# Performance work log

Hardware: AMD Instinct MI355X
Metric: run time of the kernel (lower is better)

Reference implementation:

```python
import jax, jax.numpy as jnp
import numpy as np

N, D, H, O, E = 8192, 512, 2048, 512, 8

def setup_inputs() -> dict:
    key = jax.random.key(0)
    ks = jax.random.split(key, 7)
    s = lambda *sh: 1.0 / np.sqrt(sh[-2] if len(sh) > 1 else 1.0)
    x  = jax.random.normal(ks[0], (N, D), dtype=jnp.float32)
    Wr = jax.random.normal(ks[1], (D, E), dtype=jnp.float32) * (1.0 / np.sqrt(D))
    br = jnp.zeros((E,), dtype=jnp.float32)
    W1 = jax.random.normal(ks[2], (E, D, H), dtype=jnp.float32) * (1.0 / np.sqrt(D))
    b1 = jnp.zeros((E, H), dtype=jnp.float32)
    W2 = jax.random.normal(ks[3], (E, H, O), dtype=jnp.float32) * (1.0 / np.sqrt(H))
    b2 = jnp.zeros((E, O), dtype=jnp.float32)
    return {"x": x, "Wr": Wr, "br": br, "W1": W1, "b1": b1, "W2": W2, "b2": b2}


def reference(x, Wr, br, W1, b1, W2, b2):
    # --- supervised router step: Linear -> softmax -> max ---
    router_logits = x @ Wr + br                      # [N, E]
    router_probs = jax.nn.softmax(router_logits, axis=-1)
    p_max = jnp.max(router_probs, axis=-1)           # [N]
    routes = jnp.argmax(router_probs, axis=-1)       # [N] int
    onehot = jax.nn.one_hot(routes, W1.shape[0], dtype=x.dtype)  # [N, E] dispatch mask

    # --- per-expert MLP (dense reference for the gather/compute/scatter pattern) ---
    h = jax.nn.relu(jnp.einsum('nd,edh->enh', x, W1) + b1[:, None, :])  # [E, N, H]
    all_out = jnp.einsum('enh,eho->eno', h, W2) + b2[:, None, :]        # [E, N, O]

    # --- combine: each token takes its routed expert's output ---
    out = jnp.einsum('ne,eno->no', onehot, all_out)  # [N, O]

    # straight-through scaling: value 1 in fwd, routes gradient into router probs
    scale = p_max / jax.lax.stop_gradient(p_max)
    logits = out * scale[:, None]

    counts = jnp.sum(onehot, axis=0)                 # tokens per expert
    return logits, router_probs, counts
```

## Files before the change

kernel.cpp:

```cpp
#include <hip/hip_runtime.h>
#include <hip/hip_bf16.h>
#include <stdint.h>

#define N_TOK 8192
#define DIM   512
#define HID   2048
#define OUTD  512
#define NEXP  8

typedef short  bf16x8 __attribute__((ext_vector_type(8)));
typedef float  f32x4  __attribute__((ext_vector_type(4)));
typedef unsigned short u16x8 __attribute__((ext_vector_type(8)));
typedef unsigned short u16x4 __attribute__((ext_vector_type(4)));

#define WS_CNT    0
#define WS_LIST   4096
#define WS_XBF    266240
#define WS_W1T    8654848
#define WS_W2T    25432064
#define WS_H      42209280

__device__ __forceinline__ unsigned short f2bf(float f) {
    uint32_t u = __builtin_bit_cast(uint32_t, f);
    u = (u + 0x7fffu + ((u >> 16) & 1u)) >> 16;
    return (unsigned short)u;
}

__device__ __forceinline__ void gload16(const unsigned short* g, unsigned short* l) {
    __builtin_amdgcn_global_load_lds(
        (const __attribute__((address_space(1))) unsigned int*)g,
        (__attribute__((address_space(3))) unsigned int*)l, 16, 0, 0);
}

#define MFMA_BF16 __builtin_amdgcn_mfma_f32_16x16x32_bf16

__global__ __launch_bounds__(256) void prep_kernel(
    const float* __restrict__ x, const float* __restrict__ wr, const float* __restrict__ br,
    const float* __restrict__ w1, const float* __restrict__ w2,
    float* __restrict__ probs, int* __restrict__ cnt, int* __restrict__ list,
    unsigned short* __restrict__ xbf, unsigned short* __restrict__ w1t,
    unsigned short* __restrict__ w2t)
{
    const int bid = blockIdx.x, tid = threadIdx.x;
    if (bid < 128) {
        __shared__ int lcnt[NEXP], lbase[NEXP];
        __shared__ int am_l[64], slot_l[64];
        const int w = tid >> 6, lane = tid & 63;
        if (tid < NEXP) lcnt[tid] = 0;
        __syncthreads();
        for (int i = 0; i < 16; i++) {
            const int n = bid * 64 + w * 16 + i;
            float acc[NEXP] = {};
            #pragma unroll
            for (int db = 0; db < 8; db++) {
                const int d = db * 64 + lane;
                const float xv = x[(size_t)n * DIM + d];
                const f32x4 wv0 = *(const f32x4*)&wr[d * 8];
                const f32x4 wv1 = *(const f32x4*)&wr[d * 8 + 4];
                #pragma unroll
                for (int e = 0; e < 4; e++) { acc[e] += xv * wv0[e]; acc[4 + e] += xv * wv1[e]; }
            }
            #pragma unroll
            for (int m = 1; m < 64; m <<= 1)
                #pragma unroll
                for (int e = 0; e < NEXP; e++) acc[e] += __shfl_xor(acc[e], m, 64);
            #pragma unroll
            for (int e = 0; e < NEXP; e++) acc[e] += br[e];
            float mx = acc[0]; int am = 0;
            #pragma unroll
            for (int e = 1; e < NEXP; e++) if (acc[e] > mx) { mx = acc[e]; am = e; }
            float p[NEXP]; float s = 0.f;
            #pragma unroll
            for (int e = 0; e < NEXP; e++) { p[e] = expf(acc[e] - mx); s += p[e]; }
            const float inv = 1.f / s;
            if (lane == 0) {
                f32x4 p0, p1;
                #pragma unroll
                for (int e = 0; e < 4; e++) { p0[e] = p[e] * inv; p1[e] = p[e + 4] * inv; }
                *(f32x4*)&probs[(size_t)n * NEXP]     = p0;
                *(f32x4*)&probs[(size_t)n * NEXP + 4] = p1;
                const int slot = atomicAdd(&lcnt[am], 1);
                am_l[w * 16 + i] = am; slot_l[w * 16 + i] = slot;
            }
        }
        __syncthreads();
        if (tid < NEXP) lbase[tid] = atomicAdd(&cnt[tid], lcnt[tid]);
        __syncthreads();
        if (tid < 64) {
            const int a = am_l[tid];
            list[a * N_TOK + lbase[a] + slot_l[tid]] = bid * 64 + tid;
        }
    } else if (bid < 4224) {
        __shared__ float t[64][65];
        const float* pin; unsigned short* pout; int R, C, r0, c0;
        if (bid < 2176) {
            const int loc = bid - 128, e = loc >> 8, l2 = loc & 255;
            pin = w1 + (size_t)e * DIM * HID; pout = w1t + (size_t)e * DIM * HID;
            R = DIM; C = HID; r0 = (l2 >> 5) * 64; c0 = (l2 & 31) * 64;
        } else {
            const int loc = bid - 2176, e = loc >> 8, l2 = loc & 255;
            pin = w2 + (size_t)e * HID * OUTD; pout = w2t + (size_t)e * HID * OUTD;
            R = HID; C = OUTD; r0 = (l2 >> 3) * 64; c0 = (l2 & 7) * 64;
        }
        const int r = tid >> 2, q = tid & 3;
        #pragma unroll
        for (int j = 0; j < 4; j++) {
            f32x4 v = *(const f32x4*)&pin[(size_t)(r0 + r) * C + c0 + q * 16 + j * 4];
            #pragma unroll
            for (int i = 0; i < 4; i++) t[r][q * 16 + j * 4 + i] = v[i];
        }
        __syncthreads();
        unsigned short o[16];
        #pragma unroll
        for (int i = 0; i < 16; i++) o[i] = f2bf(t[q * 16 + i][r]);
        unsigned short* dst = &pout[(size_t)(c0 + r) * R + r0 + q * 16];
        *(u16x8*)dst       = *(const u16x8*)&o[0];
        *(u16x8*)(dst + 8) = *(const u16x8*)&o[8];
    } else {
        const size_t i = (size_t)(bid - 4224) * 256 + tid;
        f32x4 a = *(const f32x4*)&x[i * 8];
        f32x4 b = *(const f32x4*)&x[i * 8 + 4];
        u16x8 o;
        #pragma unroll
        for (int j = 0; j < 4; j++) { o[j] = f2bf(a[j]); o[4 + j] = f2bf(b[j]); }
        *(u16x8*)&xbf[i * 8] = o;
    }
}

__device__ __forceinline__ int xcd_swizzle(int bid, int nwg, bool& valid) {
    const int xcd = bid & 7, cidx = bid >> 3;
    const int q = nwg >> 3, r = nwg & 7;
    const int csz = q + (xcd < r ? 1 : 0);
    valid = (cidx < csz);
    return (xcd < r ? xcd * (q + 1) : r * (q + 1) + (xcd - r) * q) + cidx;
}

__device__ __forceinline__ void tile_map128(const int* __restrict__ cnt, int tile,
                                            int& e, int& row0, int& bs, int& m_e, int& ntiles) {
    int c[NEXP]; ntiles = 0;
    #pragma unroll
    for (int i = 0; i < NEXP; i++) { c[i] = cnt[i]; ntiles += (c[i] + 127) >> 7; }
    int t = tile, b = 0, ei = 0;
    #pragma unroll
    for (int i = 0; i < NEXP; i++) {
        const int nt = (c[i] + 127) >> 7;
        if (t >= 0 && t < nt) { ei = i; row0 = t << 7; bs = b; m_e = c[i]; }
        t -= nt; b += c[i];
    }
    e = ei;
}

__global__ __launch_bounds__(256) void gemm1_kernel(
    const unsigned short* __restrict__ xbf, const unsigned short* __restrict__ w1t,
    const float* __restrict__ b1, const int* __restrict__ list,
    const int* __restrict__ cnt, unsigned short* __restrict__ h)
{
    int e = 0, row0 = 0, bs = 0, m_e = 0, ntm = 0;
    tile_map128(cnt, 0, e, row0, bs, m_e, ntm);
    const int nwg = ntm * 32;
    bool valid; const int v = xcd_swizzle(blockIdx.x, nwg, valid);
    if (!valid) return;
    const int tile = v >> 5, ntile = v & 31;
    tile_map128(cnt, tile, e, row0, bs, m_e, ntm);
    const int n0 = ntile * 64;

    __shared__ unsigned short ldsA[128 * 64] __attribute__((aligned(16)));
    __shared__ unsigned short ldsB[64 * 64]  __attribute__((aligned(16)));
    __shared__ int ldsTok[128];
    const int tid = threadIdx.x;
    if (tid < 128) { int r = row0 + tid; if (r >= m_e) r = m_e - 1; ldsTok[tid] = list[e * N_TOK + r]; }
    __syncthreads();

    const int gslot = tid & 7;
    const unsigned short* aSrc[4]; const unsigned short* bSrc[2];
    #pragma unroll
    for (int i = 0; i < 4; i++) {
        const int row = (i * 256 + tid) >> 3;
        const int col = ((gslot ^ (row & 7)) << 3);
        aSrc[i] = xbf + (size_t)ldsTok[row] * DIM + col;
    }
    #pragma unroll
    for (int i = 0; i < 2; i++) {
        const int row = (i * 256 + tid) >> 3;
        const int col = ((gslot ^ (row & 7)) << 3);
        bSrc[i] = w1t + ((size_t)e * HID + n0 + row) * DIM + col;
    }

    f32x4 acc[4][2] = {};
    const int lane = tid & 63, wid = tid >> 6;
    const int wm = (wid >> 1) * 64, wn = (wid & 1) * 32;
    const int lrow = lane & 15, gk = lane >> 4, lm = lrow & 7;

    int rowA[4], rowB[2];
    #pragma unroll
    for (int f = 0; f < 4; f++) rowA[f] = (wm + f * 16 + lrow) * 64;
    #pragma unroll
    for (int f = 0; f < 2; f++) rowB[f] = (wn + f * 16 + lrow) * 64;

    for (int t = 0; t < 8; t++) {
        const int k0 = t * 64;
        __syncthreads();
        #pragma unroll
        for (int i = 0; i < 4; i++)
            gload16(aSrc[i] + k0, ldsA + ((i << 8) + (tid & 192)) * 8);
        #pragma unroll
        for (int i = 0; i < 2; i++)
            gload16(bSrc[i] + k0, ldsB + ((i << 8) + (tid & 192)) * 8);
        __syncthreads();
        #pragma unroll
        for (int kk = 0; kk < 2; kk++) {
            bf16x8 av[4], bv[2];
            #pragma unroll
            for (int f = 0; f < 4; f++)
                av[f] = *(const bf16x8*)&ldsA[rowA[f] + ((((kk << 2) + gk) ^ lm) << 3)];
            #pragma unroll
            for (int f = 0; f < 2; f++)
                bv[f] = *(const bf16x8*)&ldsB[rowB[f] + ((((kk << 2) + gk) ^ lm) << 3)];
            #pragma unroll
            for (int mf = 0; mf < 4; mf++)
                #pragma unroll
                for (int nf = 0; nf < 2; nf++)
                    acc[mf][nf] = MFMA_BF16(av[mf], bv[nf], acc[mf][nf], 0, 0, 0);
        }
    }

    const int hbase = bs + row0;
    float bias[2];
    #pragma unroll
    for (int nf = 0; nf < 2; nf++) bias[nf] = b1[e * HID + n0 + wn + nf * 16 + lrow];
    #pragma unroll
    for (int mf = 0; mf < 4; mf++) {
        #pragma unroll
        for (int j = 0; j < 4; j++) {
            const int m = wm + mf * 16 + gk * 4 + j;
            if (row0 + m < m_e) {
                const size_t ro = (size_t)(hbase + m) * HID + n0 + wn;
                #pragma unroll
                for (int nf = 0; nf < 2; nf++) {
                    float vv = acc[mf][nf][j] + bias[nf];
                    h[ro + nf * 16 + lrow] = f2bf(vv > 0.f ? vv : 0.f);
                }
            }
        }
    }
}

__global__ __launch_bounds__(256) void gemm2_kernel(
    const unsigned short* __restrict__ h, const unsigned short* __restrict__ w2t,
    const float* __restrict__ b2, const int* __restrict__ list,
    const int* __restrict__ cnt, float* __restrict__ out, float* __restrict__ counts)
{
    const int tid = threadIdx.x;
    if (blockIdx.x == 0 && tid < NEXP) counts[tid] = (float)cnt[tid];

    int e = 0, row0 = 0, bs = 0, m_e = 0, ntm = 0;
    tile_map128(cnt, 0, e, row0, bs, m_e, ntm);
    const int nwg = ntm * 8;
    bool valid; const int v = xcd_swizzle(blockIdx.x, nwg, valid);
    if (!valid) return;
    const int tile = v >> 3, ntile = v & 7;
    tile_map128(cnt, tile, e, row0, bs, m_e, ntm);
    const int n0 = ntile * 64;

    __shared__ unsigned short ldsA[128 * 64] __attribute__((aligned(16)));
    __shared__ unsigned short ldsB[64 * 64]  __attribute__((aligned(16)));
    __shared__ int ldsTok[128];
    if (tid < 128) { int r = row0 + tid; if (r >= m_e) r = m_e - 1; ldsTok[tid] = list[e * N_TOK + r]; }
    __syncthreads();

    const int gslot = tid & 7;
    const unsigned short* aSrc[4]; const unsigned short* bSrc[2];
    #pragma unroll
    for (int i = 0; i < 4; i++) {
        const int row = (i * 256 + tid) >> 3;
        const int col = ((gslot ^ (row & 7)) << 3);
        int slot = row0 + row; if (slot >= m_e) slot = m_e - 1;
        aSrc[i] = h + (size_t)(bs + slot) * HID + col;
    }
    #pragma unroll
    for (int i = 0; i < 2; i++) {
        const int row = (i * 256 + tid) >> 3;
        const int col = ((gslot ^ (row & 7)) << 3);
        bSrc[i] = w2t + ((size_t)e * OUTD + n0 + row) * HID + col;
    }

    f32x4 acc[4][2] = {};
    const int lane = tid & 63, wid = tid >> 6;
    const int wm = (wid >> 1) * 64, wn = (wid & 1) * 32;
    const int lrow = lane & 15, gk = lane >> 4, lm = lrow & 7;

    int rowA[4], rowB[2];
    #pragma unroll
    for (int f = 0; f < 4; f++) rowA[f] = (wm + f * 16 + lrow) * 64;
    #pragma unroll
    for (int f = 0; f < 2; f++) rowB[f] = (wn + f * 16 + lrow) * 64;

    for (int t = 0; t < 32; t++) {
        const int k0 = t * 64;
        __syncthreads();
        #pragma unroll
        for (int i = 0; i < 4; i++)
            gload16(aSrc[i] + k0, ldsA + ((i << 8) + (tid & 192)) * 8);
        #pragma unroll
        for (int i = 0; i < 2; i++)
            gload16(bSrc[i] + k0, ldsB + ((i << 8) + (tid & 192)) * 8);
        __syncthreads();
        #pragma unroll
        for (int kk = 0; kk < 2; kk++) {
            bf16x8 av[4], bv[2];
            #pragma unroll
            for (int f = 0; f < 4; f++)
                av[f] = *(const bf16x8*)&ldsA[rowA[f] + ((((kk << 2) + gk) ^ lm) << 3)];
            #pragma unroll
            for (int f = 0; f < 2; f++)
                bv[f] = *(const bf16x8*)&ldsB[rowB[f] + ((((kk << 2) + gk) ^ lm) << 3)];
            #pragma unroll
            for (int mf = 0; mf < 4; mf++)
                #pragma unroll
                for (int nf = 0; nf < 2; nf++)
                    acc[mf][nf] = MFMA_BF16(av[mf], bv[nf], acc[mf][nf], 0, 0, 0);
        }
    }

    float bias[2];
    #pragma unroll
    for (int nf = 0; nf < 2; nf++) bias[nf] = b2[e * OUTD + n0 + wn + nf * 16 + lrow];
    #pragma unroll
    for (int mf = 0; mf < 4; mf++) {
        #pragma unroll
        for (int j = 0; j < 4; j++) {
            const int m = wm + mf * 16 + gk * 4 + j;
            if (row0 + m < m_e) {
                const size_t ro = (size_t)ldsTok[m] * OUTD + n0 + wn;
                #pragma unroll
                for (int nf = 0; nf < 2; nf++)
                    out[ro + nf * 16 + lrow] = acc[mf][nf][j] + bias[nf];
            }
        }
    }
}

extern "C" void kernel_launch(void* const* d_in, const int* in_sizes, int n_in,
                              void* d_out, int out_size, void* d_ws, size_t ws_size,
                              hipStream_t stream) {
    (void)in_sizes; (void)n_in; (void)out_size; (void)ws_size;
    const float* x  = (const float*)d_in[0];
    const float* wr = (const float*)d_in[1];
    const float* br = (const float*)d_in[2];
    const float* w1 = (const float*)d_in[3];
    const float* b1 = (const float*)d_in[4];
    const float* w2 = (const float*)d_in[5];
    const float* b2 = (const float*)d_in[6];

    float* out    = (float*)d_out;
    float* probs  = out + (size_t)N_TOK * OUTD;
    float* counts = probs + (size_t)N_TOK * NEXP;

    char* ws = (char*)d_ws;
    int* cnt     = (int*)(ws + WS_CNT);
    int* list    = (int*)(ws + WS_LIST);
    unsigned short* xbf = (unsigned short*)(ws + WS_XBF);
    unsigned short* w1t = (unsigned short*)(ws + WS_W1T);
    unsigned short* w2t = (unsigned short*)(ws + WS_W2T);
    unsigned short* hbf = (unsigned short*)(ws + WS_H);

    hipMemsetAsync(cnt, 0, NEXP * sizeof(int), stream);
    prep_kernel<<<6272, 256, 0, stream>>>(x, wr, br, w1, w2, probs, cnt, list, xbf, w1t, w2t);
    gemm1_kernel<<<2272, 256, 0, stream>>>(xbf, w1t, b1, list, cnt, hbf);
    gemm2_kernel<<<568, 256, 0, stream>>>(hbf, w2t, b2, list, cnt, out, counts);
}
```

Baseline: 111.7 us.

## Move W2 transpose/convert from prep kernel into gemm1 as extra blocks

```diff
diff --git a/kernel.cpp b/kernel.cpp
--- a/kernel.cpp
+++ b/kernel.cpp
@@ -36,10 +36,9 @@
 
 __global__ __launch_bounds__(256) void prep_kernel(
     const float* __restrict__ x, const float* __restrict__ wr, const float* __restrict__ br,
-    const float* __restrict__ w1, const float* __restrict__ w2,
+    const float* __restrict__ w1,
     float* __restrict__ probs, int* __restrict__ cnt, int* __restrict__ list,
-    unsigned short* __restrict__ xbf, unsigned short* __restrict__ w1t,
-    unsigned short* __restrict__ w2t)
+    unsigned short* __restrict__ xbf, unsigned short* __restrict__ w1t)
 {
     const int bid = blockIdx.x, tid = threadIdx.x;
     if (bid < 128) {
@@ -90,22 +89,16 @@
             const int a = am_l[tid];
             list[a * N_TOK + lbase[a] + slot_l[tid]] = bid * 64 + tid;
         }
-    } else if (bid < 4224) {
+    } else if (bid < 2176) {
         __shared__ float t[64][65];
-        const float* pin; unsigned short* pout; int R, C, r0, c0;
-        if (bid < 2176) {
-            const int loc = bid - 128, e = loc >> 8, l2 = loc & 255;
-            pin = w1 + (size_t)e * DIM * HID; pout = w1t + (size_t)e * DIM * HID;
-            R = DIM; C = HID; r0 = (l2 >> 5) * 64; c0 = (l2 & 31) * 64;
-        } else {
-            const int loc = bid - 2176, e = loc >> 8, l2 = loc & 255;
-            pin = w2 + (size_t)e * HID * OUTD; pout = w2t + (size_t)e * HID * OUTD;
-            R = HID; C = OUTD; r0 = (l2 >> 3) * 64; c0 = (l2 & 7) * 64;
-        }
+        const int loc = bid - 128, e = loc >> 8, l2 = loc & 255;
+        const float* pin = w1 + (size_t)e * DIM * HID;
+        unsigned short* pout = w1t + (size_t)e * DIM * HID;
+        const int r0 = (l2 >> 5) * 64, c0 = (l2 & 31) * 64;
         const int r = tid >> 2, q = tid & 3;
         #pragma unroll
         for (int j = 0; j < 4; j++) {
-            f32x4 v = *(const f32x4*)&pin[(size_t)(r0 + r) * C + c0 + q * 16 + j * 4];
+            f32x4 v = *(const f32x4*)&pin[(size_t)(r0 + r) * HID + c0 + q * 16 + j * 4];
             #pragma unroll
             for (int i = 0; i < 4; i++) t[r][q * 16 + j * 4 + i] = v[i];
         }
@@ -113,11 +106,11 @@
         unsigned short o[16];
         #pragma unroll
         for (int i = 0; i < 16; i++) o[i] = f2bf(t[q * 16 + i][r]);
-        unsigned short* dst = &pout[(size_t)(c0 + r) * R + r0 + q * 16];
+        unsigned short* dst = &pout[(size_t)(c0 + r) * DIM + r0 + q * 16];
         *(u16x8*)dst       = *(const u16x8*)&o[0];
         *(u16x8*)(dst + 8) = *(const u16x8*)&o[8];
     } else {
-        const size_t i = (size_t)(bid - 4224) * 256 + tid;
+        const size_t i = (size_t)(bid - 2176) * 256 + tid;
         f32x4 a = *(const f32x4*)&x[i * 8];
         f32x4 b = *(const f32x4*)&x[i * 8 + 4];
         u16x8 o;
@@ -150,11 +143,44 @@
     e = ei;
 }
 
+#define G1_GRID 2272
+
 __global__ __launch_bounds__(256) void gemm1_kernel(
     const unsigned short* __restrict__ xbf, const unsigned short* __restrict__ w1t,
     const float* __restrict__ b1, const int* __restrict__ list,
-    const int* __restrict__ cnt, unsigned short* __restrict__ h)
+    const int* __restrict__ cnt, unsigned short* __restrict__ h,
+    const float* __restrict__ w2, unsigned short* __restrict__ w2t)
 {
+    __shared__ char smem[25088] __attribute__((aligned(16)));
+    const int tid = threadIdx.x;
+
+    if ((int)blockIdx.x >= G1_GRID) {
+        float (*t)[65] = (float(*)[65])smem;
+        const int loc = blockIdx.x - G1_GRID, e = loc >> 8, l2 = loc & 255;
+        const float* pin = w2 + (size_t)e * HID * OUTD;
+        unsigned short* pout = w2t + (size_t)e * HID * OUTD;
+        const int r0 = (l2 >> 3) * 64, c0 = (l2 & 7) * 64;
+        const int r = tid >> 2, q = tid & 3;
+        #pragma unroll
+        for (int j = 0; j < 4; j++) {
+            f32x4 v = *(const f32x4*)&pin[(size_t)(r0 + r) * OUTD + c0 + q * 16 + j * 4];
+            #pragma unroll
+            for (int i = 0; i < 4; i++) t[r][q * 16 + j * 4 + i] = v[i];
+        }
+        __syncthreads();
+        unsigned short o[16];
+        #pragma unroll
+        for (int i = 0; i < 16; i++) o[i] = f2bf(t[q * 16 + i][r]);
+        unsigned short* dst = &pout[(size_t)(c0 + r) * HID + r0 + q * 16];
+        *(u16x8*)dst       = *(const u16x8*)&o[0];
+        *(u16x8*)(dst + 8) = *(const u16x8*)&o[8];
+        return;
+    }
+
+    unsigned short* ldsA = (unsigned short*)smem;
+    unsigned short* ldsB = (unsigned short*)(smem + 16384);
+    int* ldsTok = (int*)(smem + 24576);
+
     int e = 0, row0 = 0, bs = 0, m_e = 0, ntm = 0;
     tile_map128(cnt, 0, e, row0, bs, m_e, ntm);
     const int nwg = ntm * 32;
@@ -164,10 +190,6 @@
     tile_map128(cnt, tile, e, row0, bs, m_e, ntm);
     const int n0 = ntile * 64;
 
-    __shared__ unsigned short ldsA[128 * 64] __attribute__((aligned(16)));
-    __shared__ unsigned short ldsB[64 * 64]  __attribute__((aligned(16)));
-    __shared__ int ldsTok[128];
-    const int tid = threadIdx.x;
     if (tid < 128) { int r = row0 + tid; if (r >= m_e) r = m_e - 1; ldsTok[tid] = list[e * N_TOK + r]; }
     __syncthreads();
 
@@ -365,7 +387,7 @@
     unsigned short* hbf = (unsigned short*)(ws + WS_H);
 
     hipMemsetAsync(cnt, 0, NEXP * sizeof(int), stream);
-    prep_kernel<<<6272, 256, 0, stream>>>(x, wr, br, w1, w2, probs, cnt, list, xbf, w1t, w2t);
-    gemm1_kernel<<<2272, 256, 0, stream>>>(xbf, w1t, b1, list, cnt, hbf);
+    prep_kernel<<<4224, 256, 0, stream>>>(x, wr, br, w1, probs, cnt, list, xbf, w1t);
+    gemm1_kernel<<<G1_GRID + 2048, 256, 0, stream>>>(xbf, w1t, b1, list, cnt, hbf, w2, w2t);
     gemm2_kernel<<<568, 256, 0, stream>>>(hbf, w2t, b2, list, cnt, out, counts);
 }
```

Result: no change. 110.9 us (-0.7%).

## Fuse W1 transpose/convert into gemm1 and x conversion into router blocks

Applied to the files above, without the earlier changes.

```diff
diff --git a/kernel.cpp b/kernel.cpp
--- a/kernel.cpp
+++ b/kernel.cpp
@@ -11,12 +11,10 @@
 typedef short  bf16x8 __attribute__((ext_vector_type(8)));
 typedef float  f32x4  __attribute__((ext_vector_type(4)));
 typedef unsigned short u16x8 __attribute__((ext_vector_type(8)));
-typedef unsigned short u16x4 __attribute__((ext_vector_type(4)));
 
 #define WS_CNT    0
 #define WS_LIST   4096
 #define WS_XBF    266240
-#define WS_W1T    8654848
 #define WS_W2T    25432064
 #define WS_H      42209280
 
@@ -26,7 +24,7 @@
     return (unsigned short)u;
 }
 
-__device__ __forceinline__ void gload16(const unsigned short* g, unsigned short* l) {
+__device__ __forceinline__ void gload16(const void* g, void* l) {
     __builtin_amdgcn_global_load_lds(
         (const __attribute__((address_space(1))) unsigned int*)g,
         (__attribute__((address_space(3))) unsigned int*)l, 16, 0, 0);
@@ -34,22 +32,21 @@
 
 #define MFMA_BF16 __builtin_amdgcn_mfma_f32_16x16x32_bf16
 
-__global__ __launch_bounds__(256) void prep_kernel(
+__global__ __launch_bounds__(256) void k1_kernel(
     const float* __restrict__ x, const float* __restrict__ wr, const float* __restrict__ br,
-    const float* __restrict__ w1, const float* __restrict__ w2,
+    const float* __restrict__ w2,
     float* __restrict__ probs, int* __restrict__ cnt, int* __restrict__ list,
-    unsigned short* __restrict__ xbf, unsigned short* __restrict__ w1t,
-    unsigned short* __restrict__ w2t)
+    unsigned short* __restrict__ xbf, unsigned short* __restrict__ w2t)
 {
     const int bid = blockIdx.x, tid = threadIdx.x;
-    if (bid < 128) {
+    if (bid < 256) {
         __shared__ int lcnt[NEXP], lbase[NEXP];
-        __shared__ int am_l[64], slot_l[64];
+        __shared__ int am_l[32], slot_l[32];
         const int w = tid >> 6, lane = tid & 63;
         if (tid < NEXP) lcnt[tid] = 0;
         __syncthreads();
-        for (int i = 0; i < 16; i++) {
-            const int n = bid * 64 + w * 16 + i;
+        for (int i = 0; i < 8; i++) {
+            const int n = bid * 32 + w * 8 + i;
             float acc[NEXP] = {};
             #pragma unroll
             for (int db = 0; db < 8; db++) {
@@ -80,32 +77,38 @@
                 *(f32x4*)&probs[(size_t)n * NEXP]     = p0;
                 *(f32x4*)&probs[(size_t)n * NEXP + 4] = p1;
                 const int slot = atomicAdd(&lcnt[am], 1);
-                am_l[w * 16 + i] = am; slot_l[w * 16 + i] = slot;
+                am_l[w * 8 + i] = am; slot_l[w * 8 + i] = slot;
             }
         }
         __syncthreads();
         if (tid < NEXP) lbase[tid] = atomicAdd(&cnt[tid], lcnt[tid]);
         __syncthreads();
-        if (tid < 64) {
+        if (tid < 32) {
             const int a = am_l[tid];
-            list[a * N_TOK + lbase[a] + slot_l[tid]] = bid * 64 + tid;
-        }
-    } else if (bid < 4224) {
+            list[a * N_TOK + lbase[a] + slot_l[tid]] = bid * 32 + tid;
+        }
+        const int row = bid * 32 + (tid >> 3), seg = tid & 7;
+        const float* src = x + (size_t)row * DIM + seg * 64;
+        unsigned short* dst = xbf + (size_t)row * DIM + seg * 64;
+        #pragma unroll
+        for (int j = 0; j < 8; j++) {
+            f32x4 a = *(const f32x4*)&src[j * 8];
+            f32x4 b = *(const f32x4*)&src[j * 8 + 4];
+            u16x8 o;
+            #pragma unroll
+            for (int q2 = 0; q2 < 4; q2++) { o[q2] = f2bf(a[q2]); o[4 + q2] = f2bf(b[q2]); }
+            *(u16x8*)&dst[j * 8] = o;
+        }
+    } else {
         __shared__ float t[64][65];
-        const float* pin; unsigned short* pout; int R, C, r0, c0;
-        if (bid < 2176) {
-            const int loc = bid - 128, e = loc >> 8, l2 = loc & 255;
-            pin = w1 + (size_t)e * DIM * HID; pout = w1t + (size_t)e * DIM * HID;
-            R = DIM; C = HID; r0 = (l2 >> 5) * 64; c0 = (l2 & 31) * 64;
-        } else {
-            const int loc = bid - 2176, e = loc >> 8, l2 = loc & 255;
-            pin = w2 + (size_t)e * HID * OUTD; pout = w2t + (size_t)e * HID * OUTD;
-            R = HID; C = OUTD; r0 = (l2 >> 3) * 64; c0 = (l2 & 7) * 64;
-        }
+        const int loc = bid - 256, e = loc >> 8, l2 = loc & 255;
+        const float* pin = w2 + (size_t)e * HID * OUTD;
+        unsigned short* pout = w2t + (size_t)e * HID * OUTD;
+        const int r0 = (l2 >> 3) * 64, c0 = (l2 & 7) * 64;
         const int r = tid >> 2, q = tid & 3;
         #pragma unroll
         for (int j = 0; j < 4; j++) {
-            f32x4 v = *(const f32x4*)&pin[(size_t)(r0 + r) * C + c0 + q * 16 + j * 4];
+            f32x4 v = *(const f32x4*)&pin[(size_t)(r0 + r) * OUTD + c0 + q * 16 + j * 4];
             #pragma unroll
             for (int i = 0; i < 4; i++) t[r][q * 16 + j * 4 + i] = v[i];
         }
@@ -113,17 +116,9 @@
         unsigned short o[16];
         #pragma unroll
         for (int i = 0; i < 16; i++) o[i] = f2bf(t[q * 16 + i][r]);
-        unsigned short* dst = &pout[(size_t)(c0 + r) * R + r0 + q * 16];
+        unsigned short* dst = &pout[(size_t)(c0 + r) * HID + r0 + q * 16];
         *(u16x8*)dst       = *(const u16x8*)&o[0];
         *(u16x8*)(dst + 8) = *(const u16x8*)&o[8];
-    } else {
-        const size_t i = (size_t)(bid - 4224) * 256 + tid;
-        f32x4 a = *(const f32x4*)&x[i * 8];
-        f32x4 b = *(const f32x4*)&x[i * 8 + 4];
-        u16x8 o;
-        #pragma unroll
-        for (int j = 0; j < 4; j++) { o[j] = f2bf(a[j]); o[4 + j] = f2bf(b[j]); }
-        *(u16x8*)&xbf[i * 8] = o;
     }
 }
 
@@ -151,40 +146,41 @@
 }
 
 __global__ __launch_bounds__(256) void gemm1_kernel(
-    const unsigned short* __restrict__ xbf, const unsigned short* __restrict__ w1t,
+    const unsigned short* __restrict__ xbf, const float* __restrict__ w1,
     const float* __restrict__ b1, const int* __restrict__ list,
     const int* __restrict__ cnt, unsigned short* __restrict__ h)
 {
     int e = 0, row0 = 0, bs = 0, m_e = 0, ntm = 0;
     tile_map128(cnt, 0, e, row0, bs, m_e, ntm);
-    const int nwg = ntm * 32;
-    bool valid; const int v = xcd_swizzle(blockIdx.x, nwg, valid);
-    if (!valid) return;
-    const int tile = v >> 5, ntile = v & 31;
-    tile_map128(cnt, tile, e, row0, bs, m_e, ntm);
-    const int n0 = ntile * 64;
+    const int xcd = blockIdx.x & 7, cidx = blockIdx.x >> 3;
+    const int q = ntm >> 3, r = ntm & 7;
+    const int mts = q + (xcd < r ? 1 : 0);
+    if (cidx >= mts * 32) return;
+    const int mt0 = xcd < r ? xcd * (q + 1) : r * (q + 1) + (xcd - r) * q;
+    const int per4 = mts * 4;
+    const int ntg = cidx / per4, rem = cidx - ntg * per4;
+    const int mt = mt0 + (rem >> 2), nt = (ntg << 2) + (rem & 3);
+    tile_map128(cnt, mt, e, row0, bs, m_e, ntm);
+    const int n0 = nt * 64;
 
     __shared__ unsigned short ldsA[128 * 64] __attribute__((aligned(16)));
-    __shared__ unsigned short ldsB[64 * 64]  __attribute__((aligned(16)));
+    __shared__ float ldsT[64 * 64] __attribute__((aligned(16)));
     __shared__ int ldsTok[128];
+    unsigned short* ldsB = (unsigned short*)ldsT;
     const int tid = threadIdx.x;
-    if (tid < 128) { int r = row0 + tid; if (r >= m_e) r = m_e - 1; ldsTok[tid] = list[e * N_TOK + r]; }
+    if (tid < 128) { int rr = row0 + tid; if (rr >= m_e) rr = m_e - 1; ldsTok[tid] = list[e * N_TOK + rr]; }
     __syncthreads();
 
     const int gslot = tid & 7;
-    const unsigned short* aSrc[4]; const unsigned short* bSrc[2];
+    const unsigned short* aSrc[4];
     #pragma unroll
     for (int i = 0; i < 4; i++) {
         const int row = (i * 256 + tid) >> 3;
         const int col = ((gslot ^ (row & 7)) << 3);
         aSrc[i] = xbf + (size_t)ldsTok[row] * DIM + col;
     }
-    #pragma unroll
-    for (int i = 0; i < 2; i++) {
-        const int row = (i * 256 + tid) >> 3;
-        const int col = ((gslot ^ (row & 7)) << 3);
-        bSrc[i] = w1t + ((size_t)e * HID + n0 + row) * DIM + col;
-    }
+    const float* w1e = w1 + (size_t)e * DIM * HID + n0;
+    const int bkrow = tid >> 4, bc4 = (tid & 15) * 4;
 
     f32x4 acc[4][2] = {};
     const int lane = tid & 63, wid = tid >> 6;
@@ -195,7 +191,8 @@
     #pragma unroll
     for (int f = 0; f < 4; f++) rowA[f] = (wm + f * 16 + lrow) * 64;
     #pragma unroll
-    for (int f = 0; f < 2; f++) rowB[f] = (wn + f * 16 + lrow) * 64;
+    for (int f = 0; f < 2; f++) rowB[f] = (wn + f * 16 + lrow) * 72;
+    const int bn = tid >> 2, bq = tid & 3;
 
     for (int t = 0; t < 8; t++) {
         const int k0 = t * 64;
@@ -204,8 +201,19 @@
         for (int i = 0; i < 4; i++)
             gload16(aSrc[i] + k0, ldsA + ((i << 8) + (tid & 192)) * 8);
         #pragma unroll
-        for (int i = 0; i < 2; i++)
-            gload16(bSrc[i] + k0, ldsB + ((i << 8) + (tid & 192)) * 8);
+        for (int i = 0; i < 4; i++)
+            gload16(w1e + (size_t)(k0 + i * 16 + bkrow) * HID + bc4,
+                    (char*)ldsT + (i * 256 + tid) * 16);
+        __syncthreads();
+        float rd[16];
+        #pragma unroll
+        for (int j = 0; j < 16; j++) rd[j] = ldsT[(bq * 16 + j) * 64 + bn];
+        u16x8 o0, o1;
+        #pragma unroll
+        for (int j = 0; j < 8; j++) { o0[j] = f2bf(rd[j]); o1[j] = f2bf(rd[8 + j]); }
+        __syncthreads();
+        *(u16x8*)&ldsB[bn * 72 + bq * 16]     = o0;
+        *(u16x8*)&ldsB[bn * 72 + bq * 16 + 8] = o1;
         __syncthreads();
         #pragma unroll
         for (int kk = 0; kk < 2; kk++) {
@@ -215,7 +223,7 @@
                 av[f] = *(const bf16x8*)&ldsA[rowA[f] + ((((kk << 2) + gk) ^ lm) << 3)];
             #pragma unroll
             for (int f = 0; f < 2; f++)
-                bv[f] = *(const bf16x8*)&ldsB[rowB[f] + ((((kk << 2) + gk) ^ lm) << 3)];
+                bv[f] = *(const bf16x8*)&ldsB[rowB[f] + kk * 32 + gk * 8];
             #pragma unroll
             for (int mf = 0; mf < 4; mf++)
                 #pragma unroll
@@ -265,7 +273,7 @@
     __shared__ unsigned short ldsA[128 * 64] __attribute__((aligned(16)));
     __shared__ unsigned short ldsB[64 * 64]  __attribute__((aligned(16)));
     __shared__ int ldsTok[128];
-    if (tid < 128) { int r = row0 + tid; if (r >= m_e) r = m_e - 1; ldsTok[tid] = list[e * N_TOK + r]; }
+    if (tid < 128) { int rr = row0 + tid; if (rr >= m_e) rr = m_e - 1; ldsTok[tid] = list[e * N_TOK + rr]; }
     __syncthreads();
 
     const int gslot = tid & 7;
@@ -360,12 +368,11 @@
     int* cnt     = (int*)(ws + WS_CNT);
     int* list    = (int*)(ws + WS_LIST);
     unsigned short* xbf = (unsigned short*)(ws + WS_XBF);
-    unsigned short* w1t = (unsigned short*)(ws + WS_W1T);
     unsigned short* w2t = (unsigned short*)(ws + WS_W2T);
     unsigned short* hbf = (unsigned short*)(ws + WS_H);
 
     hipMemsetAsync(cnt, 0, NEXP * sizeof(int), stream);
-    prep_kernel<<<6272, 256, 0, stream>>>(x, wr, br, w1, w2, probs, cnt, list, xbf, w1t, w2t);
-    gemm1_kernel<<<2272, 256, 0, stream>>>(xbf, w1t, b1, list, cnt, hbf);
+    k1_kernel<<<2304, 256, 0, stream>>>(x, wr, br, w2, probs, cnt, list, xbf, w2t);
+    gemm1_kernel<<<2560, 256, 0, stream>>>(xbf, w1, b1, list, cnt, hbf);
     gemm2_kernel<<<568, 256, 0, stream>>>(hbf, w2t, b2, list, cnt, out, counts);
 }
```

Result: slower. 114.5 us (+2.5%).

## Double GEMM K-tile to 128 and fold x bf16 cast into router blocks

Applied to the files above, without the earlier changes.

```diff
diff --git a/kernel.cpp b/kernel.cpp
--- a/kernel.cpp
+++ b/kernel.cpp
@@ -11,7 +11,6 @@
 typedef short  bf16x8 __attribute__((ext_vector_type(8)));
 typedef float  f32x4  __attribute__((ext_vector_type(4)));
 typedef unsigned short u16x8 __attribute__((ext_vector_type(8)));
-typedef unsigned short u16x4 __attribute__((ext_vector_type(4)));
 
 #define WS_CNT    0
 #define WS_LIST   4096
@@ -26,7 +25,7 @@
     return (unsigned short)u;
 }
 
-__device__ __forceinline__ void gload16(const unsigned short* g, unsigned short* l) {
+__device__ __forceinline__ void gload16(const void* g, void* l) {
     __builtin_amdgcn_global_load_lds(
         (const __attribute__((address_space(1))) unsigned int*)g,
         (__attribute__((address_space(3))) unsigned int*)l, 16, 0, 0);
@@ -34,7 +33,7 @@
 
 #define MFMA_BF16 __builtin_amdgcn_mfma_f32_16x16x32_bf16
 
-__global__ __launch_bounds__(256) void prep_kernel(
+__global__ __launch_bounds__(256) void k1_kernel(
     const float* __restrict__ x, const float* __restrict__ wr, const float* __restrict__ br,
     const float* __restrict__ w1, const float* __restrict__ w2,
     float* __restrict__ probs, int* __restrict__ cnt, int* __restrict__ list,
@@ -42,14 +41,14 @@
     unsigned short* __restrict__ w2t)
 {
     const int bid = blockIdx.x, tid = threadIdx.x;
-    if (bid < 128) {
+    if (bid < 256) {
         __shared__ int lcnt[NEXP], lbase[NEXP];
-        __shared__ int am_l[64], slot_l[64];
+        __shared__ int am_l[32], slot_l[32];
         const int w = tid >> 6, lane = tid & 63;
         if (tid < NEXP) lcnt[tid] = 0;
         __syncthreads();
-        for (int i = 0; i < 16; i++) {
-            const int n = bid * 64 + w * 16 + i;
+        for (int i = 0; i < 8; i++) {
+            const int n = bid * 32 + w * 8 + i;
             float acc[NEXP] = {};
             #pragma unroll
             for (int db = 0; db < 8; db++) {
@@ -80,25 +79,37 @@
                 *(f32x4*)&probs[(size_t)n * NEXP]     = p0;
                 *(f32x4*)&probs[(size_t)n * NEXP + 4] = p1;
                 const int slot = atomicAdd(&lcnt[am], 1);
-                am_l[w * 16 + i] = am; slot_l[w * 16 + i] = slot;
+                am_l[w * 8 + i] = am; slot_l[w * 8 + i] = slot;
             }
         }
         __syncthreads();
         if (tid < NEXP) lbase[tid] = atomicAdd(&cnt[tid], lcnt[tid]);
         __syncthreads();
-        if (tid < 64) {
+        if (tid < 32) {
             const int a = am_l[tid];
-            list[a * N_TOK + lbase[a] + slot_l[tid]] = bid * 64 + tid;
-        }
-    } else if (bid < 4224) {
+            list[a * N_TOK + lbase[a] + slot_l[tid]] = bid * 32 + tid;
+        }
+        const int row = bid * 32 + (tid >> 3), seg = tid & 7;
+        const float* src = x + (size_t)row * DIM + seg * 64;
+        unsigned short* dst = xbf + (size_t)row * DIM + seg * 64;
+        #pragma unroll
+        for (int j = 0; j < 8; j++) {
+            f32x4 a = *(const f32x4*)&src[j * 8];
+            f32x4 b = *(const f32x4*)&src[j * 8 + 4];
+            u16x8 o;
+            #pragma unroll
+            for (int q2 = 0; q2 < 4; q2++) { o[q2] = f2bf(a[q2]); o[4 + q2] = f2bf(b[q2]); }
+            *(u16x8*)&dst[j * 8] = o;
+        }
+    } else {
         __shared__ float t[64][65];
-        const float* pin; unsigned short* pout; int R, C, r0, c0;
-        if (bid < 2176) {
-            const int loc = bid - 128, e = loc >> 8, l2 = loc & 255;
+        const float* pin; unsigned short* pout; int C, R, r0, c0;
+        if (bid < 2304) {
+            const int loc = bid - 256, e = loc >> 8, l2 = loc & 255;
             pin = w1 + (size_t)e * DIM * HID; pout = w1t + (size_t)e * DIM * HID;
             R = DIM; C = HID; r0 = (l2 >> 5) * 64; c0 = (l2 & 31) * 64;
         } else {
-            const int loc = bid - 2176, e = loc >> 8, l2 = loc & 255;
+            const int loc = bid - 2304, e = loc >> 8, l2 = loc & 255;
             pin = w2 + (size_t)e * HID * OUTD; pout = w2t + (size_t)e * HID * OUTD;
             R = HID; C = OUTD; r0 = (l2 >> 3) * 64; c0 = (l2 & 7) * 64;
         }
@@ -116,14 +127,6 @@
         unsigned short* dst = &pout[(size_t)(c0 + r) * R + r0 + q * 16];
         *(u16x8*)dst       = *(const u16x8*)&o[0];
         *(u16x8*)(dst + 8) = *(const u16x8*)&o[8];
-    } else {
-        const size_t i = (size_t)(bid - 4224) * 256 + tid;
-        f32x4 a = *(const f32x4*)&x[i * 8];
-        f32x4 b = *(const f32x4*)&x[i * 8 + 4];
-        u16x8 o;
-        #pragma unroll
-        for (int j = 0; j < 4; j++) { o[j] = f2bf(a[j]); o[4 + j] = f2bf(b[j]); }
-        *(u16x8*)&xbf[i * 8] = o;
     }
 }
 
@@ -149,6 +152,7 @@
     }
     e = ei;
 }
+
 
 __global__ __launch_bounds__(256) void gemm1_kernel(
     const unsigned short* __restrict__ xbf, const unsigned short* __restrict__ w1t,
@@ -164,58 +168,56 @@
     tile_map128(cnt, tile, e, row0, bs, m_e, ntm);
     const int n0 = ntile * 64;
 
-    __shared__ unsigned short ldsA[128 * 64] __attribute__((aligned(16)));
-    __shared__ unsigned short ldsB[64 * 64]  __attribute__((aligned(16)));
+    __shared__ unsigned short ldsA[128 * 128] __attribute__((aligned(16)));
+    __shared__ unsigned short ldsB[64 * 128]  __attribute__((aligned(16)));
     __shared__ int ldsTok[128];
     const int tid = threadIdx.x;
     if (tid < 128) { int r = row0 + tid; if (r >= m_e) r = m_e - 1; ldsTok[tid] = list[e * N_TOK + r]; }
     __syncthreads();
 
-    const int gslot = tid & 7;
-    const unsigned short* aSrc[4]; const unsigned short* bSrc[2];
+    const unsigned short* aSrc[8]; const unsigned short* bSrc[4];
+    #pragma unroll
+    for (int i = 0; i < 8; i++) {
+        const int g = i * 256 + tid, row = g >> 4, gc = g & 15;
+        aSrc[i] = xbf + (size_t)ldsTok[row] * DIM + ((gc ^ (row & 15)) << 3);
+    }
     #pragma unroll
     for (int i = 0; i < 4; i++) {
-        const int row = (i * 256 + tid) >> 3;
-        const int col = ((gslot ^ (row & 7)) << 3);
-        aSrc[i] = xbf + (size_t)ldsTok[row] * DIM + col;
-    }
-    #pragma unroll
-    for (int i = 0; i < 2; i++) {
-        const int row = (i * 256 + tid) >> 3;
-        const int col = ((gslot ^ (row & 7)) << 3);
-        bSrc[i] = w1t + ((size_t)e * HID + n0 + row) * DIM + col;
+        const int g = i * 256 + tid, row = g >> 4, gc = g & 15;
+        bSrc[i] = w1t + ((size_t)e * HID + n0 + row) * DIM + ((gc ^ (row & 15)) << 3);
     }
 
     f32x4 acc[4][2] = {};
     const int lane = tid & 63, wid = tid >> 6;
     const int wm = (wid >> 1) * 64, wn = (wid & 1) * 32;
-    const int lrow = lane & 15, gk = lane >> 4, lm = lrow & 7;
+    const int lrow = lane & 15, gk = lane >> 4;
 
     int rowA[4], rowB[2];
     #pragma unroll
-    for (int f = 0; f < 4; f++) rowA[f] = (wm + f * 16 + lrow) * 64;
-    #pragma unroll
-    for (int f = 0; f < 2; f++) rowB[f] = (wn + f * 16 + lrow) * 64;
-
-    for (int t = 0; t < 8; t++) {
-        const int k0 = t * 64;
-        __syncthreads();
+    for (int f = 0; f < 4; f++) rowA[f] = (wm + f * 16 + lrow) * 128;
+    #pragma unroll
+    for (int f = 0; f < 2; f++) rowB[f] = (wn + f * 16 + lrow) * 128;
+
+    for (int t = 0; t < 4; t++) {
+        const int k0 = t * 128;
+        __syncthreads();
+        #pragma unroll
+        for (int i = 0; i < 8; i++)
+            gload16(aSrc[i] + k0, ldsA + (i * 256 + tid) * 8);
         #pragma unroll
         for (int i = 0; i < 4; i++)
-            gload16(aSrc[i] + k0, ldsA + ((i << 8) + (tid & 192)) * 8);
-        #pragma unroll
-        for (int i = 0; i < 2; i++)
-            gload16(bSrc[i] + k0, ldsB + ((i << 8) + (tid & 192)) * 8);
-        __syncthreads();
-        #pragma unroll
-        for (int kk = 0; kk < 2; kk++) {
+            gload16(bSrc[i] + k0, ldsB + (i * 256 + tid) * 8);
+        __syncthreads();
+        #pragma unroll
+        for (int kk = 0; kk < 4; kk++) {
+            const int gsel = (((kk << 2) + gk) ^ lrow) << 3;
             bf16x8 av[4], bv[2];
             #pragma unroll
             for (int f = 0; f < 4; f++)
-                av[f] = *(const bf16x8*)&ldsA[rowA[f] + ((((kk << 2) + gk) ^ lm) << 3)];
+                av[f] = *(const bf16x8*)&ldsA[rowA[f] + gsel];
             #pragma unroll
             for (int f = 0; f < 2; f++)
-                bv[f] = *(const bf16x8*)&ldsB[rowB[f] + ((((kk << 2) + gk) ^ lm) << 3)];
+                bv[f] = *(const bf16x8*)&ldsB[rowB[f] + gsel];
             #pragma unroll
             for (int mf = 0; mf < 4; mf++)
                 #pragma unroll
@@ -262,58 +264,56 @@
     tile_map128(cnt, tile, e, row0, bs, m_e, ntm);
     const int n0 = ntile * 64;
 
-    __shared__ unsigned short ldsA[128 * 64] __attribute__((aligned(16)));
-    __shared__ unsigned short ldsB[64 * 64]  __attribute__((aligned(16)));
+    __shared__ unsigned short ldsA[128 * 128] __attribute__((aligned(16)));
+    __shared__ unsigned short ldsB[64 * 128]  __attribute__((aligned(16)));
     __shared__ int ldsTok[128];
     if (tid < 128) { int r = row0 + tid; if (r >= m_e) r = m_e - 1; ldsTok[tid] = list[e * N_TOK + r]; }
     __syncthreads();
 
-    const int gslot = tid & 7;
-    const unsigned short* aSrc[4]; const unsigned short* bSrc[2];
+    const unsigned short* aSrc[8]; const unsigned short* bSrc[4];
+    #pragma unroll
+    for (int i = 0; i < 8; i++) {
+        const int g = i * 256 + tid, row = g >> 4, gc = g & 15;
+        int slot = row0 + row; if (slot >= m_e) slot = m_e - 1;
+        aSrc[i] = h + (size_t)(bs + slot) * HID + ((gc ^ (row & 15)) << 3);
+    }
     #pragma unroll
     for (int i = 0; i < 4; i++) {
-        const int row = (i * 256 + tid) >> 3;
-        const int col = ((gslot ^ (row & 7)) << 3);
-        int slot = row0 + row; if (slot >= m_e) slot = m_e - 1;
-        aSrc[i] = h + (size_t)(bs + slot) * HID + col;
-    }
-    #pragma unroll
-    for (int i = 0; i < 2; i++) {
-        const int row = (i * 256 + tid) >> 3;
-        const int col = ((gslot ^ (row & 7)) << 3);
-        bSrc[i] = w2t + ((size_t)e * OUTD + n0 + row) * HID + col;
+        const int g = i * 256 + tid, row = g >> 4, gc = g & 15;
+        bSrc[i] = w2t + ((size_t)e * OUTD + n0 + row) * HID + ((gc ^ (row & 15)) << 3);
     }
 
     f32x4 acc[4][2] = {};
     const int lane = tid & 63, wid = tid >> 6;
     const int wm = (wid >> 1) * 64, wn = (wid & 1) * 32;
-    const int lrow = lane & 15, gk = lane >> 4, lm = lrow & 7;
+    const int lrow = lane & 15, gk = lane >> 4;
 
     int rowA[4], rowB[2];
     #pragma unroll
-    for (int f = 0; f < 4; f++) rowA[f] = (wm + f * 16 + lrow) * 64;
-    #pragma unroll
-    for (int f = 0; f < 2; f++) rowB[f] = (wn + f * 16 + lrow) * 64;
-
-    for (int t = 0; t < 32; t++) {
-        const int k0 = t * 64;
-        __syncthreads();
+    for (int f = 0; f < 4; f++) rowA[f] = (wm + f * 16 + lrow) * 128;
+    #pragma unroll
+    for (int f = 0; f < 2; f++) rowB[f] = (wn + f * 16 + lrow) * 128;
+
+    for (int t = 0; t < 16; t++) {
+        const int k0 = t * 128;
+        __syncthreads();
+        #pragma unroll
+        for (int i = 0; i < 8; i++)
+            gload16(aSrc[i] + k0, ldsA + (i * 256 + tid) * 8);
         #pragma unroll
         for (int i = 0; i < 4; i++)
-            gload16(aSrc[i] + k0, ldsA + ((i << 8) + (tid & 192)) * 8);
-        #pragma unroll
-        for (int i = 0; i < 2; i++)
-            gload16(bSrc[i] + k0, ldsB + ((i << 8) + (tid & 192)) * 8);
-        __syncthreads();
-        #pragma unroll
-        for (int kk = 0; kk < 2; kk++) {
+            gload16(bSrc[i] + k0, ldsB + (i * 256 + tid) * 8);
+        __syncthreads();
+        #pragma unroll
+        for (int kk = 0; kk < 4; kk++) {
+            const int gsel = (((kk << 2) + gk) ^ lrow) << 3;
             bf16x8 av[4], bv[2];
             #pragma unroll
             for (int f = 0; f < 4; f++)
-                av[f] = *(const bf16x8*)&ldsA[rowA[f] + ((((kk << 2) + gk) ^ lm) << 3)];
+                av[f] = *(const bf16x8*)&ldsA[rowA[f] + gsel];
             #pragma unroll
             for (int f = 0; f < 2; f++)
-                bv[f] = *(const bf16x8*)&ldsB[rowB[f] + ((((kk << 2) + gk) ^ lm) << 3)];
+                bv[f] = *(const bf16x8*)&ldsB[rowB[f] + gsel];
             #pragma unroll
             for (int mf = 0; mf < 4; mf++)
                 #pragma unroll
@@ -365,7 +365,7 @@
     unsigned short* hbf = (unsigned short*)(ws + WS_H);
 
     hipMemsetAsync(cnt, 0, NEXP * sizeof(int), stream);
-    prep_kernel<<<6272, 256, 0, stream>>>(x, wr, br, w1, w2, probs, cnt, list, xbf, w1t, w2t);
+    k1_kernel<<<4352, 256, 0, stream>>>(x, wr, br, w1, w2, probs, cnt, list, xbf, w1t, w2t);
     gemm1_kernel<<<2272, 256, 0, stream>>>(xbf, w1t, b1, list, cnt, hbf);
     gemm2_kernel<<<568, 256, 0, stream>>>(hbf, w2t, b2, list, cnt, out, counts);
 }
```

New measurement: 104.9 us. -6.0%, faster.
